# Kernel tuning notes

Hardware: AMD Instinct MI355X
Metric: run time of the kernel (lower is better)

## Reference

```python
import jax, jax.numpy as jnp
import numpy as np

N_LINKS = 262144
N_PAIRS = 4194304
F = 20   # feature_size
R = 20   # readout_units
T = 4    # message passing iterations


def setup_inputs() -> dict:
    key = jax.random.key(0)
    ks = jax.random.split(key, 16)
    s = 0.1
    return {
        "link_state": jax.random.normal(ks[0], (N_LINKS, F), dtype=jnp.float32),
        "first": jax.random.randint(ks[1], (N_PAIRS,), 0, N_LINKS),
        "second": jax.random.randint(ks[2], (N_PAIRS,), 0, N_LINKS),
        "state_dim": F,
        # message MLP: Linear(2F -> F)
        "W_msg": jax.random.normal(ks[3], (F, 2 * F), dtype=jnp.float32) * s,
        "b_msg": jnp.zeros((F,), dtype=jnp.float32),
        # GRUCell params (PyTorch layout: [3F, in] with r,z,n gate order)
        "W_ih": jax.random.normal(ks[4], (3 * F, F), dtype=jnp.float32) * s,
        "W_hh": jax.random.normal(ks[5], (3 * F, F), dtype=jnp.float32) * s,
        "b_ih": jnp.zeros((3 * F,), dtype=jnp.float32),
        "b_hh": jnp.zeros((3 * F,), dtype=jnp.float32),
        # readout: Linear(F->R) SELU, Linear(R->R) SELU
        "W_r1": jax.random.normal(ks[6], (R, F), dtype=jnp.float32) * s,
        "b_r1": jnp.zeros((R,), dtype=jnp.float32),
        "W_r2": jax.random.normal(ks[7], (R, R), dtype=jnp.float32) * s,
        "b_r2": jnp.zeros((R,), dtype=jnp.float32),
        # out layer: Linear(R->1)
        "W_out": jax.random.normal(ks[8], (1, R), dtype=jnp.float32) * s,
        "b_out": jnp.zeros((1,), dtype=jnp.float32),
    }


def _gru_cell(m, h, W_ih, W_hh, b_ih, b_hh):
    # PyTorch GRUCell math, gate order (r, z, n)
    gi = m @ W_ih.T + b_ih   # [N, 3F]
    gh = h @ W_hh.T + b_hh   # [N, 3F]
    i_r, i_z, i_n = jnp.split(gi, 3, axis=1)
    h_r, h_z, h_n = jnp.split(gh, 3, axis=1)
    r = jax.nn.sigmoid(i_r + h_r)
    z = jax.nn.sigmoid(i_z + h_z)
    n = jnp.tanh(i_n + r * h_n)
    return (1.0 - z) * n + z * h


def reference(link_state, first, second, state_dim,
              W_msg, b_msg, W_ih, W_hh, b_ih, b_hh,
              W_r1, b_r1, W_r2, b_r2, W_out, b_out):
    state = link_state  # [N_LINKS, F]
    for _ in range(T):
        main_edges = state[first]    # gather [N_PAIRS, F]
        neigh_edges = state[second]  # gather [N_PAIRS, F]
        edges_concat = jnp.concatenate([main_edges, neigh_edges], axis=1)
        m = jax.nn.selu(edges_concat @ W_msg.T + b_msg)  # [N_PAIRS, F]
        agg = jnp.zeros_like(state).at[second].add(m)    # scatter_add back to links
        state = _gru_cell(agg, state, W_ih, W_hh, b_ih, b_hh)
    feature = jnp.sum(state, axis=0)  # [F]
    h1 = jax.nn.selu(W_r1 @ feature + b_r1)
    h2 = jax.nn.selu(W_r2 @ h1 + b_r2)
    return W_out @ h2 + b_out  # [1]
```

## Files before the change

### kernel.cpp

```cpp
#include <hip/hip_runtime.h>
#include <hip/hip_fp16.h>

#define N_LINKS 262144
#define N_PAIRS 4194304
#define F 20
#define XB 20
#define T_ITERS 4

#define NSB 256
#define LPS 1024
#define PB 256
#define PT 1024
#define PCHUNK (N_PAIRS / PB)
#define PPT (PCHUNK / PT)

typedef float f32x2 __attribute__((ext_vector_type(2)));
typedef _Float16 h16x2 __attribute__((ext_vector_type(2)));

__device__ __forceinline__ float selu_f(float x) {
    const float scale = 1.0507009873554805f;
    const float scale_alpha = 1.7580993408473766f;
    return x > 0.0f ? scale * x : scale_alpha * (__expf(x) - 1.0f);
}

__device__ __forceinline__ float selu_b(float x) {
    const float s = 1.0507009873554805f;
    const float sa = 1.7580993408473766f;
    const float mx = fmaxf(x, 0.0f);
    const float mn = fminf(x, 0.0f);
    return fmaf(sa, __expf(mn), fmaf(s, mx, -sa));
}

__device__ __forceinline__ float sigmoid_f(float x) {
    return 1.0f / (1.0f + __expf(-x));
}

__device__ __forceinline__ float tanh_fast(float x) {
    x = fminf(fmaxf(x, -15.0f), 15.0f);
    float e = __expf(2.0f * x);
    return (e - 1.0f) / (e + 1.0f);
}

__device__ __forceinline__ void store_row_fp8(unsigned char* rowp, const float* o1) {
    int* p = (int*)rowp;
#pragma unroll
    for (int i = 0; i < 5; ++i) {
        int w = 0;
        w = __builtin_amdgcn_cvt_pk_fp8_f32(o1[4*i+0], o1[4*i+1], w, false);
        w = __builtin_amdgcn_cvt_pk_fp8_f32(o1[4*i+2], o1[4*i+3], w, true);
        p[i] = w;
    }
}


__global__ void __launch_bounds__(PT)
k_part(const int* __restrict__ first, const int* __restrict__ second,
       int* __restrict__ ent, int* __restrict__ ptable, int* __restrict__ sectot) {
    __shared__ int hist[NSB];
    __shared__ int cur[NSB];
    const int b = blockIdx.x;
    const int cbase = b * PCHUNK;
    const int tid = threadIdx.x;
    for (int i = tid; i < NSB; i += PT) hist[i] = 0;
    __syncthreads();
    int sv[PPT];
#pragma unroll
    for (int k = 0; k < PPT; ++k) {
        sv[k] = second[cbase + k * PT + tid];
        atomicAdd(&hist[sv[k] >> 10], 1);
    }
    __syncthreads();
    if (tid < NSB) {
        int acc = 0;
        for (int j = 0; j < tid; ++j) acc += hist[j];
        cur[tid] = acc;
        ptable[b * (NSB + 1) + tid] = acc;
        if (tid == 0) ptable[b * (NSB + 1) + NSB] = PCHUNK;
        atomicAdd(&sectot[tid], hist[tid]);
    }
    __syncthreads();
#pragma unroll
    for (int k = 0; k < PPT; ++k) {
        const int s = sv[k];
        const int f = first[cbase + k * PT + tid];
        const int pos = atomicAdd(&cur[s >> 10], 1);
        ent[cbase + pos] = f | ((s & 1023) << 18);
    }
}

__global__ void k_scan256(const int* __restrict__ sectot, int* __restrict__ sbase,
                          int* __restrict__ rs) {
    __shared__ int s[NSB];
    const int t = threadIdx.x;
    s[t] = sectot[t];
    __syncthreads();
    if (t == 0) {
        int acc = 0;
        for (int j = 0; j < NSB; ++j) { int c = s[j]; s[j] = acc; acc += c; }
    }
    __syncthreads();
    sbase[t] = s[t];
    if (t == 0) { sbase[NSB] = N_PAIRS; rs[N_LINKS] = N_PAIRS; }
}

__global__ void __launch_bounds__(PT)
k_build(const int* __restrict__ ptable, const int* __restrict__ sbase,
        const int* __restrict__ ent, int* __restrict__ srcs, int* __restrict__ rs,
        int* __restrict__ lid) {
    __shared__ int rstart[PB];
    __shared__ int rlen[PB];
    __shared__ int lcnt[LPS];
    __shared__ int cur[LPS];
    __shared__ int dhist[64];
    __shared__ int dbase[64];
    __shared__ int dcur[64];
    const int sb = blockIdx.x;
    const int tid = threadIdx.x;
    if (tid < PB) {
        const int o0 = ptable[tid * (NSB + 1) + sb];
        const int o1 = ptable[tid * (NSB + 1) + sb + 1];
        rstart[tid] = tid * PCHUNK + o0;
        rlen[tid] = o1 - o0;
    }
    lcnt[tid] = 0;
    if (tid < 64) { dhist[tid] = 0; dcur[tid] = 0; }
    __syncthreads();
    const int wave = tid >> 6;
    const int lane = tid & 63;
    for (int j = wave; j < PB; j += (PT >> 6)) {
        const int r0 = rstart[j], rl = rlen[j];
        for (int i = lane; i < rl; i += 64)
            atomicAdd(&lcnt[(ent[r0 + i] >> 18) & 1023], 1);
    }
    __syncthreads();
    const int count = lcnt[tid];
    const int dbin = min(count, 63);
    atomicAdd(&dhist[dbin], 1);
    __syncthreads();
    if (tid == 0) {
        int acc = 0;
        for (int b = 0; b < 64; ++b) { dbase[b] = acc; acc += dhist[b]; }
    }
    __syncthreads();
    const int rank = dbase[dbin] + atomicAdd(&dcur[dbin], 1);
    lcnt[rank] = count;
    lid[sb * LPS + rank] = sb * LPS + tid;
    __syncthreads();
    for (int off = 1; off < LPS; off <<= 1) {
        const int v = (tid >= off) ? lcnt[tid - off] : 0;
        __syncthreads();
        lcnt[tid] += v;
        __syncthreads();
    }
    const int sbb = sbase[sb];
    const int excl = lcnt[rank] - count;
    rs[sb * LPS + rank] = sbb + excl;
    cur[tid] = excl;
    __syncthreads();
    for (int j = wave; j < PB; j += (PT >> 6)) {
        const int r0 = rstart[j], rl = rlen[j];
        for (int i = lane; i < rl; i += 64) {
            const int e = ent[r0 + i];
            const int pos = atomicAdd(&cur[(e >> 18) & 1023], 1);
            srcs[sbb + pos] = (e & 0x3FFFF) * 20;
        }
    }
}


__global__ void k_premsg(const float* __restrict__ state,
                         const float* __restrict__ W_msg,
                         const float* __restrict__ b_msg,
                         unsigned char* __restrict__ X1b, __half* __restrict__ X2h) {
    __shared__ float Wl[F * 2 * F];
    __shared__ float bl[F];
    for (int i = threadIdx.x; i < F * 2 * F; i += blockDim.x) Wl[i] = W_msg[i];
    if (threadIdx.x < F) bl[threadIdx.x] = b_msg[threadIdx.x];
    __syncthreads();

    int l = blockIdx.x * blockDim.x + threadIdx.x;

    float s[F];
    const float4* sp = (const float4*)(state + (size_t)l * F);
#pragma unroll
    for (int i = 0; i < 5; ++i) {
        float4 v = sp[i];
        s[4*i+0] = v.x; s[4*i+1] = v.y; s[4*i+2] = v.z; s[4*i+3] = v.w;
    }
    float o1[F], o2[F];
#pragma unroll
    for (int o = 0; o < F; ++o) {
        float a1 = bl[o], a2 = 0.0f;
#pragma unroll
        for (int k = 0; k < F; ++k) {
            a1 = fmaf(Wl[o * 2 * F + k],     s[k], a1);
            a2 = fmaf(Wl[o * 2 * F + F + k], s[k], a2);
        }
        o1[o] = a1; o2[o] = a2;
    }
    store_row_fp8(X1b + (size_t)l * XB, o1);
    __half2* xp = (__half2*)(X2h + (size_t)l * F);
#pragma unroll
    for (int i = 0; i < 10; ++i)
        xp[i] = __halves2half2(__float2half(o2[2*i]), __float2half(o2[2*i+1]));
}

__global__ void __launch_bounds__(256)
k_agg(const int* __restrict__ rs, const int* __restrict__ lid,
      const int* __restrict__ srcs,
      const unsigned char* __restrict__ X1b, const __half* __restrict__ X2h,
      float* __restrict__ agg) {
    const int wave = threadIdx.x >> 6;
    const int lane = threadIdx.x & 63;
    const int g = lane / 10;
    const int j = lane - g * 10;
    const int gsel = (g < 6) ? g : 5;
    const int slot = (blockIdx.x * 4 + wave) * 6 + gsel;

    const bool active = (g < 6) && (slot < N_LINKS);
    const int sc = min(slot, N_LINKS - 1);
    const int link = lid[sc];
    const int row_start = rs[sc];
    const int cnt = active ? (rs[sc + 1] - row_start) : 0;
    const int cl = (cnt > 0) ? (cnt - 1) : 0;

    const __half2 hv = *(const __half2*)(X2h + (size_t)link * F + 2 * j);
    const float x2a = __half2float(__low2half(hv));
    const float x2b = __half2float(__high2half(hv));

    int cmax = cnt;
#pragma unroll
    for (int off = 1; off < 64; off <<= 1)
        cmax = max(cmax, __shfl_xor(cmax, off, 64));

    float acc_a = 0.0f, acc_b = 0.0f;

    for (int base = 0; base < cmax; base += 10) {
        const int sv = srcs[row_start + min(base + j, cl)];
#pragma unroll
        for (int r = 0; r < 10; ++r) {
            const int src = __shfl(sv, gsel * 10 + r, 64);
            const unsigned v = *(const unsigned short*)(X1b + src + 2 * j);
            const f32x2 xx = __builtin_amdgcn_cvt_pk_f32_fp8((int)v, false);
            const bool ok = (base + r) < cnt;
            acc_a += ok ? selu_b(xx[0] + x2a) : 0.0f;
            acc_b += ok ? selu_b(xx[1] + x2b) : 0.0f;
        }
    }
    if (active) {
        float2 o; o.x = acc_a; o.y = acc_b;
        *(float2*)(agg + (size_t)link * F + 2 * j) = o;
    }
}

__global__ void __launch_bounds__(256)
k_gru(const float* __restrict__ agg, const float* __restrict__ h_in,
      const float* __restrict__ W_ih, const float* __restrict__ W_hh,
      const float* __restrict__ b_ih, const float* __restrict__ b_hh,
      const float* __restrict__ W_msg, const float* __restrict__ b_msg,
      float* __restrict__ h_out, unsigned char* __restrict__ X1b,
      __half* __restrict__ X2h, float* __restrict__ feature, int flags) {
    __shared__ h16x2 WiH[3 * F * 10];
    __shared__ h16x2 WhH[3 * F * 10];
    __shared__ h16x2 WmH[F * 20];
    __shared__ float bi[3 * F];
    __shared__ float bh[3 * F];
    __shared__ float bm[F];
    __shared__ float red[4 * F];
    {
        _Float16* wi = (_Float16*)WiH;
        _Float16* wh = (_Float16*)WhH;
        for (int i = threadIdx.x; i < 3 * F * F; i += blockDim.x) {
            wi[i] = (_Float16)W_ih[i];
            wh[i] = (_Float16)W_hh[i];
        }
        _Float16* wm = (_Float16*)WmH;
        for (int i = threadIdx.x; i < F * 2 * F; i += blockDim.x)
            wm[i] = (_Float16)W_msg[i];
    }
    if (threadIdx.x < 3 * F) {
        bi[threadIdx.x] = b_ih[threadIdx.x];
        bh[threadIdx.x] = b_hh[threadIdx.x];
    }
    if (threadIdx.x < F) bm[threadIdx.x] = b_msg[threadIdx.x];
    __syncthreads();

    const int l = blockIdx.x * blockDim.x + threadIdx.x;

    float m[F], h[F];
    const float4* mp = (const float4*)(agg  + (size_t)l * F);
    const float4* hp = (const float4*)(h_in + (size_t)l * F);
#pragma unroll
    for (int i = 0; i < 5; ++i) {
        float4 vm = mp[i], vh = hp[i];
        m[4*i+0] = vm.x; m[4*i+1] = vm.y; m[4*i+2] = vm.z; m[4*i+3] = vm.w;
        h[4*i+0] = vh.x; h[4*i+1] = vh.y; h[4*i+2] = vh.z; h[4*i+3] = vh.w;
    }
    h16x2 mh[10], hh[10];
#pragma unroll
    for (int i = 0; i < 10; ++i) {
        mh[i][0] = (_Float16)m[2*i]; mh[i][1] = (_Float16)m[2*i+1];
        hh[i][0] = (_Float16)h[2*i]; hh[i][1] = (_Float16)h[2*i+1];
    }

    float hn[F];
#pragma unroll
    for (int j = 0; j < F; ++j) {
        float gri = 0.f, gzi = 0.f, gin = bi[2*F + j];
        float grh = 0.f, gzh = 0.f, ghn = bh[2*F + j];
#pragma unroll
        for (int k = 0; k < 10; ++k) {
            gri = __builtin_amdgcn_fdot2(WiH[(0*F + j) * 10 + k], mh[k], gri, false);
            gzi = __builtin_amdgcn_fdot2(WiH[(1*F + j) * 10 + k], mh[k], gzi, false);
            gin = __builtin_amdgcn_fdot2(WiH[(2*F + j) * 10 + k], mh[k], gin, false);
            grh = __builtin_amdgcn_fdot2(WhH[(0*F + j) * 10 + k], hh[k], grh, false);
            gzh = __builtin_amdgcn_fdot2(WhH[(1*F + j) * 10 + k], hh[k], gzh, false);
            ghn = __builtin_amdgcn_fdot2(WhH[(2*F + j) * 10 + k], hh[k], ghn, false);
        }
        float r = sigmoid_f(bi[j] + bh[j] + gri + grh);
        float z = sigmoid_f(bi[F + j] + bh[F + j] + gzi + gzh);
        float n = tanh_fast(gin + r * ghn);
        hn[j] = (1.0f - z) * n + z * h[j];
    }

    float4* op = (float4*)(h_out + (size_t)l * F);
#pragma unroll
    for (int i = 0; i < 5; ++i)
        op[i] = make_float4(hn[4*i], hn[4*i+1], hn[4*i+2], hn[4*i+3]);

    if (flags & 1) {
        h16x2 hnh[10];
#pragma unroll
        for (int i = 0; i < 10; ++i) {
            hnh[i][0] = (_Float16)hn[2*i]; hnh[i][1] = (_Float16)hn[2*i+1];
        }
        float o1[F], o2[F];
#pragma unroll
        for (int o = 0; o < F; ++o) {
            float a1 = bm[o], a2 = 0.0f;
#pragma unroll
            for (int k = 0; k < 10; ++k) {
                a1 = __builtin_amdgcn_fdot2(WmH[o * 20 + k],      hnh[k], a1, false);
                a2 = __builtin_amdgcn_fdot2(WmH[o * 20 + 10 + k], hnh[k], a2, false);
            }
            o1[o] = a1; o2[o] = a2;
        }
        store_row_fp8(X1b + (size_t)l * XB, o1);
        __half2* xp = (__half2*)(X2h + (size_t)l * F);
#pragma unroll
        for (int i = 0; i < 10; ++i)
            xp[i] = __halves2half2(__float2half(o2[2*i]), __float2half(o2[2*i+1]));
    }

    if (flags & 2) {
#pragma unroll
        for (int off = 1; off < 64; off <<= 1) {
#pragma unroll
            for (int j = 0; j < F; ++j) hn[j] += __shfl_xor(hn[j], off, 64);
        }
        const int lane = threadIdx.x & 63;
        const int wave = threadIdx.x >> 6;
        if (lane == 0) {
#pragma unroll
            for (int j = 0; j < F; ++j) red[wave * F + j] = hn[j];
        }
        __syncthreads();
        if (threadIdx.x < F) {
            float s = red[threadIdx.x] + red[F + threadIdx.x] +
                      red[2 * F + threadIdx.x] + red[3 * F + threadIdx.x];
            atomicAdd(&feature[threadIdx.x], s);
        }
    }
}

__global__ void k_readout(const float* __restrict__ feature,
                          const float* __restrict__ W_r1, const float* __restrict__ b_r1,
                          const float* __restrict__ W_r2, const float* __restrict__ b_r2,
                          const float* __restrict__ W_out, const float* __restrict__ b_out,
                          float* __restrict__ out) {
    if (threadIdx.x != 0 || blockIdx.x != 0) return;
    float fv[F], h1[F], h2[F];
#pragma unroll
    for (int i = 0; i < F; ++i) fv[i] = feature[i];
#pragma unroll
    for (int o = 0; o < F; ++o) {
        float a = b_r1[o];
#pragma unroll
        for (int k = 0; k < F; ++k) a = fmaf(W_r1[o * F + k], fv[k], a);
        h1[o] = selu_f(a);
    }
#pragma unroll
    for (int o = 0; o < F; ++o) {
        float a = b_r2[o];
#pragma unroll
        for (int k = 0; k < F; ++k) a = fmaf(W_r2[o * F + k], h1[k], a);
        h2[o] = selu_f(a);
    }
    float a = b_out[0];
#pragma unroll
    for (int k = 0; k < F; ++k) a = fmaf(W_out[k], h2[k], a);
    out[0] = a;
}

extern "C" void kernel_launch(void* const* d_in, const int* in_sizes, int n_in,
                              void* d_out, int out_size, void* d_ws, size_t ws_size,
                              hipStream_t stream) {
    const float* link_state = (const float*)d_in[0];
    const int*   first      = (const int*)  d_in[1];
    const int*   second     = (const int*)  d_in[2];
    const float* W_msg = (const float*)d_in[4];
    const float* b_msg = (const float*)d_in[5];
    const float* W_ih  = (const float*)d_in[6];
    const float* W_hh  = (const float*)d_in[7];
    const float* b_ih  = (const float*)d_in[8];
    const float* b_hh  = (const float*)d_in[9];
    const float* W_r1  = (const float*)d_in[10];
    const float* b_r1  = (const float*)d_in[11];
    const float* W_r2  = (const float*)d_in[12];
    const float* b_r2  = (const float*)d_in[13];
    const float* W_out = (const float*)d_in[14];
    const float* b_out = (const float*)d_in[15];
    float* out = (float*)d_out;

    const size_t NF = (size_t)N_LINKS * F;
    float* state   = (float*)d_ws;
    float* agg     = state + NF;
    unsigned char* X1b = (unsigned char*)(agg + NF);
    __half* X2h    = (__half*)(X1b + (size_t)N_LINKS * XB + 64);
    int*    srcs   = (int*)(X2h + NF);
    int*    rs     = srcs + N_PAIRS;
    int*    lid    = rs + N_LINKS + 1;
    float* feature = (float*)(lid + N_LINKS);
    int* ptable    = (int*)(feature + 32);
    int* sectot    = ptable + PB * (NSB + 1);
    int* sbase     = sectot + NSB;
    int* ent       = (int*)agg;

    hipMemsetAsync(sectot, 0, NSB * sizeof(int), stream);
    hipMemsetAsync(feature, 0, F * sizeof(float), stream);

    k_part<<<PB, PT, 0, stream>>>(first, second, ent, ptable, sectot);
    k_scan256<<<1, NSB, 0, stream>>>(sectot, sbase, rs);
    k_build<<<NSB, PT, 0, stream>>>(ptable, sbase, ent, srcs, rs, lid);

    k_premsg<<<N_LINKS / 256, 256, 0, stream>>>(link_state, W_msg, b_msg, X1b, X2h);
    const int aggBlocks = (N_LINKS + 23) / 24;
    for (int t = 0; t < T_ITERS; ++t) {
        const float* h = (t == 0) ? link_state : state;
        int flags = (t < T_ITERS - 1 ? 1 : 0) | (t == T_ITERS - 1 ? 2 : 0);
        k_agg<<<aggBlocks, 256, 0, stream>>>(rs, lid, srcs, X1b, X2h, agg);
        k_gru<<<N_LINKS / 256, 256, 0, stream>>>(agg, h, W_ih, W_hh, b_ih, b_hh,
                                                 W_msg, b_msg, state, X1b, X2h,
                                                 feature, flags);
    }
    k_readout<<<1, 64, 0, stream>>>(feature, W_r1, b_r1, W_r2, b_r2, W_out, b_out, out);
}
```

Baseline: 584.9 us.

## Renumber links into sorted-slot order so aggregation reads and writes contiguously

Builds an inverse permutation from the sorted link order and remaps each pair's source index into slot space. State, X1b, X2h and agg are then all stored in slot order, so k_agg no longer goes through lid and its reads of X2h and writes of agg are contiguous. k_premsg gathers the initial link_state into slot order once. This adds two setup kernels (inverse permutation and remap over all pairs) and an extra state copy, in exchange for removing the scattered per-link accesses in every iteration. The final feature sum does not depend on ordering, so the result is unchanged.

Result: slower. 601.3 us (+2.8%).

```diff
diff --git a/kernel.cpp b/kernel.cpp
--- a/kernel.cpp
+++ b/kernel.cpp
@@ -162,29 +162,44 @@
         for (int i = lane; i < rl; i += 64) {
             const int e = ent[r0 + i];
             const int pos = atomicAdd(&cur[(e >> 18) & 1023], 1);
-            srcs[sbb + pos] = (e & 0x3FFFF) * 20;
-        }
-    }
-}
-
-
-__global__ void k_premsg(const float* __restrict__ state,
+            srcs[sbb + pos] = e & 0x3FFFF;
+        }
+    }
+}
+
+__global__ void k_inv(const int* __restrict__ lid, int* __restrict__ rnk) {
+    const int i = blockIdx.x * blockDim.x + threadIdx.x;
+    rnk[lid[i]] = i;
+}
+
+__global__ void k_remap(int* __restrict__ srcs, const int* __restrict__ rnk) {
+    const int p = blockIdx.x * blockDim.x + threadIdx.x;
+    srcs[p] = rnk[srcs[p]] * 20;
+}
+
+
+__global__ void k_premsg(const float* __restrict__ link_state,
+                         const int* __restrict__ lid,
                          const float* __restrict__ W_msg,
                          const float* __restrict__ b_msg,
-                         unsigned char* __restrict__ X1b, __half* __restrict__ X2h) {
+                         unsigned char* __restrict__ X1b, __half* __restrict__ X2h,
+                         float* __restrict__ state_r) {
     __shared__ float Wl[F * 2 * F];
     __shared__ float bl[F];
     for (int i = threadIdx.x; i < F * 2 * F; i += blockDim.x) Wl[i] = W_msg[i];
     if (threadIdx.x < F) bl[threadIdx.x] = b_msg[threadIdx.x];
     __syncthreads();
 
-    int l = blockIdx.x * blockDim.x + threadIdx.x;
+    const int slot = blockIdx.x * blockDim.x + threadIdx.x;
+    const int link = lid[slot];
 
     float s[F];
-    const float4* sp = (const float4*)(state + (size_t)l * F);
+    const float4* sp = (const float4*)(link_state + (size_t)link * F);
+    float4* so = (float4*)(state_r + (size_t)slot * F);
 #pragma unroll
     for (int i = 0; i < 5; ++i) {
         float4 v = sp[i];
+        so[i] = v;
         s[4*i+0] = v.x; s[4*i+1] = v.y; s[4*i+2] = v.z; s[4*i+3] = v.w;
     }
     float o1[F], o2[F];
@@ -198,16 +213,15 @@
         }
         o1[o] = a1; o2[o] = a2;
     }
-    store_row_fp8(X1b + (size_t)l * XB, o1);
-    __half2* xp = (__half2*)(X2h + (size_t)l * F);
+    store_row_fp8(X1b + (size_t)slot * XB, o1);
+    __half2* xp = (__half2*)(X2h + (size_t)slot * F);
 #pragma unroll
     for (int i = 0; i < 10; ++i)
         xp[i] = __halves2half2(__float2half(o2[2*i]), __float2half(o2[2*i+1]));
 }
 
 __global__ void __launch_bounds__(256)
-k_agg(const int* __restrict__ rs, const int* __restrict__ lid,
-      const int* __restrict__ srcs,
+k_agg(const int* __restrict__ rs, const int* __restrict__ srcs,
       const unsigned char* __restrict__ X1b, const __half* __restrict__ X2h,
       float* __restrict__ agg) {
     const int wave = threadIdx.x >> 6;
@@ -219,12 +233,11 @@
 
     const bool active = (g < 6) && (slot < N_LINKS);
     const int sc = min(slot, N_LINKS - 1);
-    const int link = lid[sc];
     const int row_start = rs[sc];
     const int cnt = active ? (rs[sc + 1] - row_start) : 0;
     const int cl = (cnt > 0) ? (cnt - 1) : 0;
 
-    const __half2 hv = *(const __half2*)(X2h + (size_t)link * F + 2 * j);
+    const __half2 hv = *(const __half2*)(X2h + (size_t)sc * F + 2 * j);
     const float x2a = __half2float(__low2half(hv));
     const float x2b = __half2float(__high2half(hv));
 
@@ -249,7 +262,7 @@
     }
     if (active) {
         float2 o; o.x = acc_a; o.y = acc_b;
-        *(float2*)(agg + (size_t)link * F + 2 * j) = o;
+        *(float2*)(agg + (size_t)slot * F + 2 * j) = o;
     }
 }
 
@@ -430,7 +443,8 @@
     int*    srcs   = (int*)(X2h + NF);
     int*    rs     = srcs + N_PAIRS;
     int*    lid    = rs + N_LINKS + 1;
-    float* feature = (float*)(lid + N_LINKS);
+    int*    rnk    = lid + N_LINKS;
+    float* feature = (float*)(rnk + N_LINKS);
     int* ptable    = (int*)(feature + 32);
     int* sectot    = ptable + PB * (NSB + 1);
     int* sbase     = sectot + NSB;
@@ -442,14 +456,16 @@
     k_part<<<PB, PT, 0, stream>>>(first, second, ent, ptable, sectot);
     k_scan256<<<1, NSB, 0, stream>>>(sectot, sbase, rs);
     k_build<<<NSB, PT, 0, stream>>>(ptable, sbase, ent, srcs, rs, lid);
-
-    k_premsg<<<N_LINKS / 256, 256, 0, stream>>>(link_state, W_msg, b_msg, X1b, X2h);
+    k_inv<<<N_LINKS / 256, 256, 0, stream>>>(lid, rnk);
+    k_remap<<<N_PAIRS / 256, 256, 0, stream>>>(srcs, rnk);
+
+    k_premsg<<<N_LINKS / 256, 256, 0, stream>>>(link_state, lid, W_msg, b_msg,
+                                                X1b, X2h, state);
     const int aggBlocks = (N_LINKS + 23) / 24;
     for (int t = 0; t < T_ITERS; ++t) {
-        const float* h = (t == 0) ? link_state : state;
         int flags = (t < T_ITERS - 1 ? 1 : 0) | (t == T_ITERS - 1 ? 2 : 0);
-        k_agg<<<aggBlocks, 256, 0, stream>>>(rs, lid, srcs, X1b, X2h, agg);
-        k_gru<<<N_LINKS / 256, 256, 0, stream>>>(agg, h, W_ih, W_hh, b_ih, b_hh,
+        k_agg<<<aggBlocks, 256, 0, stream>>>(rs, srcs, X1b, X2h, agg);
+        k_gru<<<N_LINKS / 256, 256, 0, stream>>>(agg, state, W_ih, W_hh, b_ih, b_hh,
                                                  W_msg, b_msg, state, X1b, X2h,
                                                  feature, flags);
     }
```
